# Kernel tuning notes

Hardware: AMD Instinct MI355X
Metric: run time of the kernel (lower is better)

Reference implementation:

```python
import jax, jax.numpy as jnp
import numpy as np

BLOCK = 2  # block_size from init_kwargs


def setup_inputs() -> dict:
    key = jax.random.key(0)
    inputs = jax.random.normal(key, (4, 32, 64, 64, 128), dtype=jnp.float32)
    return {"inputs": inputs}


def reference(inputs) -> jnp.ndarray:
    # 3D depth_to_space, channels_last.
    # The original builds b**3 sparse ConvTransposes with diagonal one-hot
    # filters, gathers channel slices, and add_n's. That reduces exactly to:
    #   out[n, z*b+dz, y*b+dy, x*b+dx, c] = in[n, z, y, x, i*Cout + c]
    # with i = row-major flatten of (dz, dy, dx).
    b = BLOCK
    B, D, H, W, C = inputs.shape
    Co = C // (b ** 3)
    x = inputs.reshape(B, D, H, W, b, b, b, Co)          # split channels -> (dz,dy,dx,Co)
    x = x.transpose(0, 1, 4, 2, 5, 3, 6, 7)              # (B, D, dz, H, dy, W, dx, Co)
    return x.reshape(B, D * b, H * b, W * b, Co)
```

## Files before the change

### kernel.cpp

```cpp
#include <hip/hip_runtime.h>


typedef float f32x4 __attribute__((ext_vector_type(4)));

__global__ __launch_bounds__(256) void d2s_kernel(const f32x4* __restrict__ in4,
                                                  f32x4* __restrict__ out4) {
    constexpr unsigned int N4 = 16777216u;
    constexpr unsigned int STRIDE = N4 / 4u;
    unsigned int base = blockIdx.x * 256u + threadIdx.x;

#pragma unroll
    for (int it = 0; it < 4; ++it) {
        unsigned int idx = base + (unsigned int)it * STRIDE;

        unsigned int c4 = idx & 3u;
        unsigned int t  = idx >> 2;
        unsigned int X  = t & 127u;  t >>= 7;
        unsigned int Y  = t & 127u;  t >>= 7;
        unsigned int Z  = t & 63u;
        unsigned int n  = t >> 6;

        unsigned int x = X >> 1, dx = X & 1u;
        unsigned int y = Y >> 1, dy = Y & 1u;
        unsigned int z = Z >> 1, dz = Z & 1u;
        unsigned int i = dz * 4u + dy * 2u + dx;

        unsigned int in_idx = ((((n * 32u + z) * 64u + y) * 64u + x) << 5) + (i << 2) + c4;

        out4[idx] = in4[in_idx];
    }
}

extern "C" void kernel_launch(void* const* d_in, const int* in_sizes, int n_in,
                              void* d_out, int out_size, void* d_ws, size_t ws_size,
                              hipStream_t stream) {
    const f32x4* in4 = (const f32x4*)d_in[0];
    f32x4* out4 = (f32x4*)d_out;
    int block = 256;
    int grid = 16384;
    d2s_kernel<<<grid, block, 0, stream>>>(in4, out4);
}
```

Before: 118.0 us.

## Stage depth-to-space rows through swizzled LDS for fully coalesced reads and writes

Each block loads one contiguous input row (all x and channels for a fixed n,z,y) into shared memory with an XOR swizzle. It then writes the four corresponding output rows (dz,dy) contiguously. This replaces the per-element gather with 64-byte input runs by fully contiguous loads and stores. The cost is 32KB of LDS per block, a barrier, and lower occupancy.

```diff
diff --git a/kernel.cpp b/kernel.cpp
--- a/kernel.cpp
+++ b/kernel.cpp
@@ -3,31 +3,48 @@
 
 typedef float f32x4 __attribute__((ext_vector_type(4)));
 
-__global__ __launch_bounds__(256) void d2s_kernel(const f32x4* __restrict__ in4,
-                                                  f32x4* __restrict__ out4) {
-    constexpr unsigned int N4 = 16777216u;
-    constexpr unsigned int STRIDE = N4 / 4u;
-    unsigned int base = blockIdx.x * 256u + threadIdx.x;
+__global__ __launch_bounds__(256) void d2s_lds(const f32x4* __restrict__ in4,
+                                               f32x4* __restrict__ out4) {
+    __shared__ f32x4 lds[2048];
+
+    unsigned int b = blockIdx.x;
+    unsigned int t = threadIdx.x;
+    unsigned int n = b >> 11;
+    unsigned int z = (b >> 6) & 31u;
+    unsigned int y = b & 63u;
+
+    const f32x4* src = in4 + ((size_t)b << 11);
+
+    f32x4 v[8];
+#pragma unroll
+    for (int j = 0; j < 8; ++j) v[j] = src[t + 256u * j];
 
 #pragma unroll
-    for (int it = 0; it < 4; ++it) {
-        unsigned int idx = base + (unsigned int)it * STRIDE;
+    for (int j = 0; j < 8; ++j) {
+        unsigned int p = t + 256u * j;
+        unsigned int x = p >> 5;
+        unsigned int s = p & 31u;
+        lds[(x << 5) | (s ^ (x & 31u))] = v[j];
+    }
+    __syncthreads();
 
-        unsigned int c4 = idx & 3u;
-        unsigned int t  = idx >> 2;
-        unsigned int X  = t & 127u;  t >>= 7;
-        unsigned int Y  = t & 127u;  t >>= 7;
-        unsigned int Z  = t & 63u;
-        unsigned int n  = t >> 6;
+    unsigned int Zb = z << 1, Yb = y << 1;
+#pragma unroll
+    for (int j = 0; j < 8; ++j) {
+        unsigned int q = t + 256u * j;
+        unsigned int r = q >> 9;
+        unsigned int rem = q & 511u;
+        unsigned int c4 = rem & 3u;
+        unsigned int X = rem >> 2;
+        unsigned int x = X >> 1, dx = X & 1u;
+        unsigned int i = (r << 1) | dx;
+        unsigned int s = (i << 2) | c4;
+        f32x4 val = lds[(x << 5) | (s ^ (x & 31u))];
 
-        unsigned int x = X >> 1, dx = X & 1u;
-        unsigned int y = Y >> 1, dy = Y & 1u;
-        unsigned int z = Z >> 1, dz = Z & 1u;
-        unsigned int i = dz * 4u + dy * 2u + dx;
-
-        unsigned int in_idx = ((((n * 32u + z) * 64u + y) * 64u + x) << 5) + (i << 2) + c4;
-
-        out4[idx] = in4[in_idx];
+        unsigned int Z = Zb + (r >> 1);
+        unsigned int Y = Yb + (r & 1u);
+        unsigned int oidx = ((((n << 6) + Z) << 7) + Y);
+        out4[((size_t)oidx << 9) + rem] = val;
     }
 }
 
@@ -37,6 +54,6 @@
     const f32x4* in4 = (const f32x4*)d_in[0];
     f32x4* out4 = (f32x4*)d_out;
     int block = 256;
-    int grid = 16384;
-    d2s_kernel<<<grid, block, 0, stream>>>(in4, out4);
+    int grid = 8192;
+    d2s_lds<<<grid, block, 0, stream>>>(in4, out4);
 }
```

Result: faster. 98.99 us (-16.1%).
